# Kernel tuning notes

Measured on AMD Instinct MI355X. Metric: run time of the kernel, lower is better.

The kernel has to match this reference:

```python
import jax, jax.numpy as jnp
import numpy as np

K = 5  # per_pix_kernel


def spatial_attention(x, w):
    # x: [N, k^2, H, W]; w: [1, 2, 7, 7] conv weight, padding=3, no bias
    avg = jnp.mean(x, axis=1, keepdims=True)
    mx = jnp.max(x, axis=1, keepdims=True)
    s = jnp.concatenate([avg, mx], axis=1)  # [N,2,H,W]
    y = jax.lax.conv_general_dilated(
        s, w, window_strides=(1, 1), padding=[(3, 3), (3, 3)],
        dimension_numbers=('NCHW', 'OIHW', 'NCHW'))
    return jax.nn.sigmoid(y)  # [N,1,H,W]


def fac(feat, filters, k):
    # feat: [N,C,H,W]; filters: [N,k^2,H,W] per-pixel kernel shared across channels
    N, C, H, W = feat.shape
    pad = (k - 1) // 2
    p = jnp.pad(feat, ((0, 0), (0, 0), (pad, pad), (pad, pad)))
    # patches[n,c,h,w,s] with s = kh*k + kw (matches torch unfold(2).unfold(3) row-major order)
    patches = jnp.stack([p[:, :, i:i + H, j:j + W]
                         for i in range(k) for j in range(k)], axis=-1)
    return jnp.einsum('nchws,nshw->nchw', patches, filters)


def setup_inputs() -> dict:
    key = jax.random.key(0)
    ks = jax.random.split(key, 7)
    N, C, H, W = 16, 3, 256, 256
    return {
        'blur_info': jax.random.normal(ks[0], (N, C, H, W), jnp.float32),
        'perpix_1': jax.random.normal(ks[1], (N, K * K, H, W), jnp.float32),
        'perpix_2': jax.random.normal(ks[2], (N, K * K, H, W), jnp.float32),
        'perpix_3': jax.random.normal(ks[3], (N, K * K, H, W), jnp.float32),
        'w1': jax.random.normal(ks[4], (1, 2, 7, 7), jnp.float32) * 0.1,
        'w2': jax.random.normal(ks[5], (1, 2, 7, 7), jnp.float32) * 0.1,
        'w3': jax.random.normal(ks[6], (1, 2, 7, 7), jnp.float32) * 0.1,
    }


def reference(blur_info, perpix_1, perpix_2, perpix_3, w1, w2, w3):
    perpix = [perpix_1, perpix_2, perpix_3]
    weights = [w1, w2, w3]
    reblur = []
    for pk, w in zip(perpix, weights):
        mask = spatial_attention(pk, w)            # [N,1,H,W]
        sharp = blur_info * (1.0 - mask)
        blur = fac(blur_info * mask, pk, K)        # per-pixel adaptive filtering
        reblur.append(sharp + blur)
    out = reblur[0]
    for r in reblur[1:]:
        out = out + r
    return out / len(reblur)
```

## Files before the change

kernel.cpp:

```cpp
#include <hip/hip_runtime.h>

#define NIMG 16
#define NC 3
#define H 256
#define W 256
#define HW (H * W)
#define NS 25
#define TH 32
#define TW 32
#define SRH (TH + 10)
#define SRW (TW + 10)
#define MRH (TH + 4)
#define MRW (TW + 4)
#define NTHREADS 256
#define PPT ((TH * TW) / NTHREADS)

__device__ __forceinline__ unsigned bf16r(float x) {
    union { float f; unsigned u; } c; c.f = x;
    return (c.u + 0x7FFFu + ((c.u >> 16) & 1u)) >> 16;
}
__device__ __forceinline__ float bf_hi(unsigned u) {
    union { unsigned u; float f; } c; c.u = u & 0xFFFF0000u; return c.f;
}
__device__ __forceinline__ float bf_lo(unsigned u) {
    union { unsigned u; float f; } c; c.u = u << 16; return c.f;
}

__global__ __launch_bounds__(256)
void reduce_s(const float* __restrict__ pp, unsigned* __restrict__ s_ws) {
    const int n   = blockIdx.y;
    const int pix = blockIdx.x * 256 + threadIdx.x;
    const float* p = pp + n * (NS * HW) + pix;
    float v = p[0];
    float sum = v, mx = v;
    #pragma unroll
    for (int s = 1; s < NS; ++s) {
        float x = p[s * HW];
        sum += x; mx = fmaxf(mx, x);
    }
    s_ws[n * HW + pix] = (bf16r(sum) << 16) | bf16r(mx);
}

__global__ __launch_bounds__(NTHREADS)
void reblur_bc(const float* __restrict__ blur_info,
               const float* __restrict__ pp,
               const unsigned* __restrict__ s_ws,
               const float* __restrict__ wt,
               float* __restrict__ out,
               int first)
{
    __shared__ unsigned s_l[SRH * SRW];
    __shared__ float q[NC][MRH * MRW];
    __shared__ float wts[98];

    const int tid = threadIdx.x;
    const int n  = blockIdx.z;
    const int h0 = blockIdx.y * TH;
    const int w0 = blockIdx.x * TW;

    for (int i = tid; i < 98; i += NTHREADS)
        wts[i] = wt[i] * (i < 49 ? 0.04f : 1.0f);

    for (int i = tid; i < SRH * SRW; i += NTHREADS) {
        int rr = i / SRW, cc = i % SRW;
        int gh = h0 - 5 + rr, gw = w0 - 5 + cc;
        unsigned u = 0;
        if ((unsigned)gh < H && (unsigned)gw < W)
            u = s_ws[n * HW + gh * W + gw];
        s_l[i] = u;
    }
    __syncthreads();

    for (int i = tid; i < MRH * MRW; i += NTHREADS) {
        int rr = i / MRW, cc = i % MRW;
        float a = 0.f;
        #pragma unroll
        for (int j = 0; j < 7; ++j) {
            #pragma unroll
            for (int t = 0; t < 7; ++t) {
                unsigned u = s_l[(rr + j) * SRW + cc + t];
                a += bf_hi(u) * wts[j * 7 + t] + bf_lo(u) * wts[49 + j * 7 + t];
            }
        }
        float m = 1.f / (1.f + __expf(-a));
        int gh = h0 - 2 + rr, gw = w0 - 2 + cc;
        bool inb = (unsigned)gh < H && (unsigned)gw < W;
        int gi = gh * W + gw;
        #pragma unroll
        for (int c = 0; c < NC; ++c) {
            float bv = inb ? blur_info[(n * NC + c) * HW + gi] : 0.f;
            q[c][i] = m * bv;
        }
    }
    __syncthreads();

    const float inv3 = 1.f / 3.f;
    for (int k = 0; k < PPT; ++k) {
        int oi = tid + k * NTHREADS;
        int r = oi / TW, cc = oi % TW;
        const float* pk = pp + n * (NS * HW) + (h0 + r) * W + (w0 + cc);
        int qc = (r + 2) * MRW + cc + 2;
        float f0 = -q[0][qc], f1 = -q[1][qc], f2 = -q[2][qc];
        #pragma unroll
        for (int s = 0; s < NS; ++s) {
            const int qi = (r + s / 5) * MRW + cc + (s % 5);
            float v = pk[s * HW];
            f0 += v * q[0][qi];
            f1 += v * q[1][qi];
            f2 += v * q[2][qi];
        }
        int gi = (h0 + r) * W + (w0 + cc);
        if (first) {
            out[(n * NC + 0) * HW + gi] = blur_info[(n * NC + 0) * HW + gi] + f0 * inv3;
            out[(n * NC + 1) * HW + gi] = blur_info[(n * NC + 1) * HW + gi] + f1 * inv3;
            out[(n * NC + 2) * HW + gi] = blur_info[(n * NC + 2) * HW + gi] + f2 * inv3;
        } else {
            out[(n * NC + 0) * HW + gi] += f0 * inv3;
            out[(n * NC + 1) * HW + gi] += f1 * inv3;
            out[(n * NC + 2) * HW + gi] += f2 * inv3;
        }
    }
}

extern "C" void kernel_launch(void* const* d_in, const int* in_sizes, int n_in,
                              void* d_out, int out_size, void* d_ws, size_t ws_size,
                              hipStream_t stream) {
    const float* blur = (const float*)d_in[0];
    float* out = (float*)d_out;
    unsigned* s_ws = (unsigned*)d_ws;

    dim3 gridA(HW / 256, NIMG);
    dim3 gridB(W / TW, H / TH, NIMG);

    for (int b = 0; b < 3; ++b) {
        const float* pp = (const float*)d_in[1 + b];
        const float* wt = (const float*)d_in[4 + b];
        reduce_s<<<gridA, 256, 0, stream>>>(pp, s_ws);
        reblur_bc<<<gridB, NTHREADS, 0, stream>>>(blur, pp, s_ws, wt, out, b == 0);
    }
}
```

Before: 394.8 us.

## Fuse channel reduction, attention and filtering for all three branches into one kernel

Replaces the per-branch reduce kernel plus reblur kernel pair with a single kernel that computes the mean/max reduction directly over the tile's halo region, then runs the attention conv and per-pixel filtering for all three branches. Results accumulate in registers and the output is written once. This removes the workspace round trip, the repeated read-modify-write of the output, and five kernel launches. In exchange, halo pixels of the reduction are recomputed redundantly across tiles and register pressure rises.

```diff
diff --git a/kernel.cpp b/kernel.cpp
--- a/kernel.cpp
+++ b/kernel.cpp
@@ -10,10 +10,13 @@
 #define TW 32
 #define SRH (TH + 10)
 #define SRW (TW + 10)
+#define SRN (SRH * SRW)
 #define MRH (TH + 4)
 #define MRW (TW + 4)
+#define MRN (MRH * MRW)
 #define NTHREADS 256
 #define PPT ((TH * TW) / NTHREADS)
+#define RPT ((SRN + NTHREADS - 1) / NTHREADS)
 
 __device__ __forceinline__ unsigned bf16r(float x) {
     union { float f; unsigned u; } c; c.f = x;
@@ -26,99 +29,126 @@
     union { unsigned u; float f; } c; c.u = u << 16; return c.f;
 }
 
-__global__ __launch_bounds__(256)
-void reduce_s(const float* __restrict__ pp, unsigned* __restrict__ s_ws) {
-    const int n   = blockIdx.y;
-    const int pix = blockIdx.x * 256 + threadIdx.x;
-    const float* p = pp + n * (NS * HW) + pix;
-    float v = p[0];
-    float sum = v, mx = v;
-    #pragma unroll
-    for (int s = 1; s < NS; ++s) {
-        float x = p[s * HW];
-        sum += x; mx = fmaxf(mx, x);
-    }
-    s_ws[n * HW + pix] = (bf16r(sum) << 16) | bf16r(mx);
-}
-
-__global__ __launch_bounds__(NTHREADS)
-void reblur_bc(const float* __restrict__ blur_info,
-               const float* __restrict__ pp,
-               const unsigned* __restrict__ s_ws,
-               const float* __restrict__ wt,
-               float* __restrict__ out,
-               int first)
+__global__ __launch_bounds__(NTHREADS, 4)
+void reblur_fused(const float* __restrict__ blur_info,
+                  const float* __restrict__ pp0,
+                  const float* __restrict__ pp1,
+                  const float* __restrict__ pp2,
+                  const float* __restrict__ wt0,
+                  const float* __restrict__ wt1,
+                  const float* __restrict__ wt2,
+                  float* __restrict__ out)
 {
-    __shared__ unsigned s_l[SRH * SRW];
-    __shared__ float q[NC][MRH * MRW];
-    __shared__ float wts[98];
+    __shared__ unsigned s_l[SRN];
+    __shared__ float q[NC][MRN];
+    __shared__ float wts[3][98];
 
     const int tid = threadIdx.x;
     const int n  = blockIdx.z;
     const int h0 = blockIdx.y * TH;
     const int w0 = blockIdx.x * TW;
 
-    for (int i = tid; i < 98; i += NTHREADS)
-        wts[i] = wt[i] * (i < 49 ? 0.04f : 1.0f);
+    if (tid < 98) {
+        float sc = (tid < 49) ? 0.04f : 1.0f;
+        wts[0][tid] = wt0[tid] * sc;
+        wts[1][tid] = wt1[tid] * sc;
+        wts[2][tid] = wt2[tid] * sc;
+    }
 
-    for (int i = tid; i < SRH * SRW; i += NTHREADS) {
-        int rr = i / SRW, cc = i % SRW;
+    int off[RPT]; bool val[RPT];
+    #pragma unroll
+    for (int r = 0; r < RPT; ++r) {
+        int rp = tid + r * NTHREADS;
+        int rr = rp / SRW, cc = rp % SRW;
         int gh = h0 - 5 + rr, gw = w0 - 5 + cc;
-        unsigned u = 0;
-        if ((unsigned)gh < H && (unsigned)gw < W)
-            u = s_ws[n * HW + gh * W + gw];
-        s_l[i] = u;
+        val[r] = (rp < SRN) && ((unsigned)gh < H) && ((unsigned)gw < W);
+        off[r] = gh * W + gw;
     }
-    __syncthreads();
 
-    for (int i = tid; i < MRH * MRW; i += NTHREADS) {
-        int rr = i / MRW, cc = i % MRW;
-        float a = 0.f;
+    float facc0[PPT], facc1[PPT], facc2[PPT];
+    #pragma unroll
+    for (int k = 0; k < PPT; ++k) { facc0[k] = 0.f; facc1[k] = 0.f; facc2[k] = 0.f; }
+
+    const size_t nbase = (size_t)n * NS * HW;
+
+    #pragma unroll 1
+    for (int b = 0; b < 3; ++b) {
+        const float* pb = (b == 0) ? pp0 : ((b == 1) ? pp1 : pp2);
+        pb += nbase;
+
+        float sm[RPT], mx[RPT];
         #pragma unroll
-        for (int j = 0; j < 7; ++j) {
+        for (int r = 0; r < RPT; ++r) { sm[r] = 0.f; mx[r] = -3.0e38f; }
+        #pragma unroll 5
+        for (int s = 0; s < NS; ++s) {
+            const float* pl = pb + s * HW;
             #pragma unroll
-            for (int t = 0; t < 7; ++t) {
-                unsigned u = s_l[(rr + j) * SRW + cc + t];
-                a += bf_hi(u) * wts[j * 7 + t] + bf_lo(u) * wts[49 + j * 7 + t];
+            for (int r = 0; r < RPT; ++r) {
+                float v = val[r] ? pl[off[r]] : 0.f;
+                sm[r] += v;
+                mx[r] = fmaxf(mx[r], v);
             }
         }
-        float m = 1.f / (1.f + __expf(-a));
-        int gh = h0 - 2 + rr, gw = w0 - 2 + cc;
-        bool inb = (unsigned)gh < H && (unsigned)gw < W;
-        int gi = gh * W + gw;
         #pragma unroll
-        for (int c = 0; c < NC; ++c) {
-            float bv = inb ? blur_info[(n * NC + c) * HW + gi] : 0.f;
-            q[c][i] = m * bv;
+        for (int r = 0; r < RPT; ++r) {
+            int rp = tid + r * NTHREADS;
+            if (rp < SRN)
+                s_l[rp] = val[r] ? ((bf16r(sm[r]) << 16) | bf16r(mx[r])) : 0u;
+        }
+        __syncthreads();
+
+        const float* wb = &wts[b][0];
+        for (int i = tid; i < MRN; i += NTHREADS) {
+            int rr = i / MRW, cc = i % MRW;
+            float a = 0.f;
+            #pragma unroll
+            for (int j = 0; j < 7; ++j) {
+                #pragma unroll
+                for (int t = 0; t < 7; ++t) {
+                    unsigned u = s_l[(rr + j) * SRW + cc + t];
+                    a += bf_hi(u) * wb[j * 7 + t] + bf_lo(u) * wb[49 + j * 7 + t];
+                }
+            }
+            float m = 1.f / (1.f + __expf(-a));
+            int gh = h0 - 2 + rr, gw = w0 - 2 + cc;
+            bool inb = (unsigned)gh < H && (unsigned)gw < W;
+            int gi = gh * W + gw;
+            #pragma unroll
+            for (int c = 0; c < NC; ++c) {
+                float bv = inb ? blur_info[(n * NC + c) * HW + gi] : 0.f;
+                q[c][i] = m * bv;
+            }
+        }
+        __syncthreads();
+
+        #pragma unroll
+        for (int k = 0; k < PPT; ++k) {
+            int oi = tid + k * NTHREADS;
+            int r = oi / TW, cc = oi % TW;
+            const float* pk = pb + (h0 + r) * W + (w0 + cc);
+            int qc = (r + 2) * MRW + cc + 2;
+            float f0 = -q[0][qc], f1 = -q[1][qc], f2 = -q[2][qc];
+            #pragma unroll
+            for (int s = 0; s < NS; ++s) {
+                int qi = (r + s / 5) * MRW + cc + (s % 5);
+                float v = pk[s * HW];
+                f0 += v * q[0][qi];
+                f1 += v * q[1][qi];
+                f2 += v * q[2][qi];
+            }
+            facc0[k] += f0; facc1[k] += f1; facc2[k] += f2;
         }
     }
-    __syncthreads();
 
     const float inv3 = 1.f / 3.f;
+    #pragma unroll
     for (int k = 0; k < PPT; ++k) {
         int oi = tid + k * NTHREADS;
         int r = oi / TW, cc = oi % TW;
-        const float* pk = pp + n * (NS * HW) + (h0 + r) * W + (w0 + cc);
-        int qc = (r + 2) * MRW + cc + 2;
-        float f0 = -q[0][qc], f1 = -q[1][qc], f2 = -q[2][qc];
-        #pragma unroll
-        for (int s = 0; s < NS; ++s) {
-            const int qi = (r + s / 5) * MRW + cc + (s % 5);
-            float v = pk[s * HW];
-            f0 += v * q[0][qi];
-            f1 += v * q[1][qi];
-            f2 += v * q[2][qi];
-        }
         int gi = (h0 + r) * W + (w0 + cc);
-        if (first) {
-            out[(n * NC + 0) * HW + gi] = blur_info[(n * NC + 0) * HW + gi] + f0 * inv3;
-            out[(n * NC + 1) * HW + gi] = blur_info[(n * NC + 1) * HW + gi] + f1 * inv3;
-            out[(n * NC + 2) * HW + gi] = blur_info[(n * NC + 2) * HW + gi] + f2 * inv3;
-        } else {
-            out[(n * NC + 0) * HW + gi] += f0 * inv3;
-            out[(n * NC + 1) * HW + gi] += f1 * inv3;
-            out[(n * NC + 2) * HW + gi] += f2 * inv3;
-        }
+        out[(n * NC + 0) * HW + gi] = blur_info[(n * NC + 0) * HW + gi] + facc0[k] * inv3;
+        out[(n * NC + 1) * HW + gi] = blur_info[(n * NC + 1) * HW + gi] + facc1[k] * inv3;
+        out[(n * NC + 2) * HW + gi] = blur_info[(n * NC + 2) * HW + gi] + facc2[k] * inv3;
     }
 }
 
@@ -127,15 +157,11 @@
                               hipStream_t stream) {
     const float* blur = (const float*)d_in[0];
     float* out = (float*)d_out;
-    unsigned* s_ws = (unsigned*)d_ws;
 
-    dim3 gridA(HW / 256, NIMG);
-    dim3 gridB(W / TW, H / TH, NIMG);
-
-    for (int b = 0; b < 3; ++b) {
-        const float* pp = (const float*)d_in[1 + b];
-        const float* wt = (const float*)d_in[4 + b];
-        reduce_s<<<gridA, 256, 0, stream>>>(pp, s_ws);
-        reblur_bc<<<gridB, NTHREADS, 0, stream>>>(blur, pp, s_ws, wt, out, b == 0);
-    }
+    dim3 grid(W / TW, H / TH, NIMG);
+    reblur_fused<<<grid, NTHREADS, 0, stream>>>(
+        blur,
+        (const float*)d_in[1], (const float*)d_in[2], (const float*)d_in[3],
+        (const float*)d_in[4], (const float*)d_in[5], (const float*)d_in[6],
+        out);
 }
```

After: 419.4 us. +6.2%, slower.
